# Kernel optimization log

Hardware: AMD Instinct MI355X
Metric: run time of the kernel (lower is better)

The kernel has to match this reference:

```python
import jax, jax.numpy as jnp
import numpy as np

DEPTH = 4
EPS = 1e-5


def block_pool(x, g):
    # adaptive max pool over a g x g grid of blocks, broadcast back to full size.
    # Equivalent to the recursive HalfSplit/adaptive_max_pool2d/QuarterStitch pyramid.
    B, C, H, W = x.shape
    xr = x.reshape(B, C, g, H // g, g, W // g)
    m = xr.max(axis=(3, 5), keepdims=True)          # [B,C,g,1,g,1]
    return jnp.broadcast_to(m, xr.shape).reshape(B, C, H, W)


def conv1x1_bn(x, w, gamma, beta):
    # Conv2DNormed: 1x1 conv (no bias) followed by BatchNorm (batch statistics).
    y = jnp.einsum('bchw,oc->bohw', x, w)
    mu = y.mean(axis=(0, 2, 3), keepdims=True)
    var = y.var(axis=(0, 2, 3), keepdims=True)
    yhat = (y - mu) * jax.lax.rsqrt(var + EPS)
    return yhat * gamma[None, :, None, None] + beta[None, :, None, None]


def setup_inputs() -> dict:
    key = jax.random.key(0)
    k0, k1, k2 = jax.random.split(key, 3)
    B, C, H, W = 4, 256, 192, 192
    x = jax.random.normal(k0, (B, C, H, W), jnp.float32)
    ws = jax.random.normal(k1, (DEPTH, C, C), jnp.float32) / np.float32(np.sqrt(C))
    gs = jnp.ones((DEPTH, C), jnp.float32)
    bs = jnp.zeros((DEPTH, C), jnp.float32)
    wf = jax.random.normal(k2, (C, (DEPTH + 1) * C), jnp.float32) / np.float32(np.sqrt((DEPTH + 1) * C))
    gf = jnp.ones((C,), jnp.float32)
    bf = jnp.zeros((C,), jnp.float32)
    return {"x": x, "ws": ws, "gs": gs, "bs": bs, "wf": wf, "gf": gf, "bf": bf}


def reference(x, ws, gs, bs, wf, gf, bf):
    # p[0] = raw input; p[1+d] = conv_d(block-pooled input at grid 2^d), d=0..DEPTH-1
    p = [x]
    for d in range(DEPTH):
        pooled = block_pool(x, 2 ** d)
        p.append(conv1x1_bn(pooled, ws[d], gs[d], bs[d]))
    out = jnp.concatenate(p, axis=1)                # [B, (DEPTH+1)*C, H, W]
    return conv1x1_bn(out, wf, gf, bf)
```

## Files before the change

### kernel.cpp

```cpp
#include <hip/hip_runtime.h>

typedef unsigned short u16;
typedef unsigned int   u32;
typedef __attribute__((ext_vector_type(4))) float f32x4;
typedef __attribute__((ext_vector_type(8))) short s16x8;
typedef __attribute__((ext_vector_type(4))) unsigned short u16x4;

#define HW    36864
#define WPIX  192
#define NCH   256
#define NB    4
#define NPIX  147456
#define POS   85
#define BN_EPS 1e-5f
#define NBKT  16

#define WS_PALL    0
#define WS_YD      (WS_PALL + NB*NCH*POS)
#define WS_PSUM    (WS_YD + NB*NCH*POS)
#define WS_PSQ     (WS_PSUM + 1024)
#define WS_PSC     (WS_PSQ + 1024)
#define WS_PBI     (WS_PSC + 1024)
#define WS_CONTRIB (WS_PBI + 1024)
#define WS_FSUMB   (WS_CONTRIB + NB*NCH*64)
#define WS_FSQB    (WS_FSUMB + NBKT*256)
#define WS_FSC     (WS_FSQB + NBKT*256)
#define WS_FBI     (WS_FSC + 256)
#define WS_WPK     (WS_FBI + 256)
#define WS_YBF     (WS_WPK + 32768)
#define WS_YBF_FLOATS (NB*NCH*HW/2)
#define WS_TOTAL   (WS_YBF + WS_YBF_FLOATS)

__device__ __forceinline__ u16 f2bf(float f) {
  u32 u = __builtin_bit_cast(u32, f);
  u += 0x7fffu + ((u >> 16) & 1u);
  return (u16)(u >> 16);
}
__device__ __forceinline__ float bf2f(u16 h) {
  u32 u = ((u32)h) << 16;
  return __builtin_bit_cast(float, u);
}

__global__ __launch_bounds__(192) void k_pool(const float* __restrict__ x, float* __restrict__ wsb) {
  __shared__ float sm[8][4][48];
  __shared__ float sp[84];
  int bc = blockIdx.x;
  const float* base = x + (size_t)bc * HW;
  int t = threadIdx.x;
  int cg = t % 48, rg = t / 48;
  if (bc == 0) {
    for (int i = t; i < 2048; i += 192) wsb[WS_PSUM + i] = 0.f;
    for (int i = t; i < 2*NBKT*256; i += 192) wsb[WS_FSUMB + i] = 0.f;
  }
  #pragma unroll
  for (int byi = 0; byi < 8; byi++) {
    float mm = -3.4e38f;
    #pragma unroll
    for (int rr = 0; rr < 6; rr++) {
      int r = byi*24 + rg + 4*rr;
      f32x4 v = *(const f32x4*)(base + r*WPIX + cg*4);
      mm = fmaxf(mm, fmaxf(fmaxf(v.x, v.y), fmaxf(v.z, v.w)));
    }
    sm[byi][rg][cg] = mm;
  }
  __syncthreads();
  size_t pb = WS_PALL + (size_t)bc * POS;
  if (t < 64) {
    int by = t >> 3, bx = t & 7;
    float mm = -3.4e38f;
    for (int r2 = 0; r2 < 4; r2++)
      for (int cq = 0; cq < 6; cq++)
        mm = fmaxf(mm, sm[by][r2][bx*6 + cq]);
    sp[t] = mm;
    wsb[pb + t] = mm;
  }
  __syncthreads();
  if (t < 16) {
    int i = t >> 2, j = t & 3;
    float mm = fmaxf(fmaxf(sp[(2*i)*8 + 2*j], sp[(2*i)*8 + 2*j + 1]),
                     fmaxf(sp[(2*i+1)*8 + 2*j], sp[(2*i+1)*8 + 2*j + 1]));
    sp[64 + t] = mm;
    wsb[pb + 64 + t] = mm;
  }
  __syncthreads();
  if (t < 4) {
    int i = t >> 1, j = t & 1;
    float mm = fmaxf(fmaxf(sp[64 + (2*i)*4 + 2*j], sp[64 + (2*i)*4 + 2*j + 1]),
                     fmaxf(sp[64 + (2*i+1)*4 + 2*j], sp[64 + (2*i+1)*4 + 2*j + 1]));
    sp[80 + t] = mm;
    wsb[pb + 80 + t] = mm;
  }
  __syncthreads();
  if (t == 0)
    wsb[pb + 84] = fmaxf(fmaxf(sp[80], sp[81]), fmaxf(sp[82], sp[83]));
}

__global__ __launch_bounds__(256) void k_wpack(const float* __restrict__ wf, float* __restrict__ wsb) {
  int fid = blockIdx.x*256 + threadIdx.x;
  int m = fid & 255, g = (fid >> 8) & 3, ks = fid >> 10;
  const float* src = wf + (size_t)m*1280 + ks*32 + g*8;
  f32x4 a = *(const f32x4*)src;
  f32x4 c = *(const f32x4*)(src + 4);
  u32* dst = (u32*)((u16*)(wsb + WS_WPK) + (size_t)fid*8);
  dst[0] = (u32)f2bf(a.x) | ((u32)f2bf(a.y) << 16);
  dst[1] = (u32)f2bf(a.z) | ((u32)f2bf(a.w) << 16);
  dst[2] = (u32)f2bf(c.x) | ((u32)f2bf(c.y) << 16);
  dst[3] = (u32)f2bf(c.z) | ((u32)f2bf(c.w) << 16);
}

__global__ __launch_bounds__(256) void k_pyr(const float* __restrict__ wconv, float* __restrict__ wsb) {
  __shared__ __align__(16) float pv[256];
  int bi = blockIdx.x;
  int b = bi / 85, pos = bi % 85;
  int d = (pos < 64) ? 3 : (pos < 80) ? 2 : (pos < 84) ? 1 : 0;
  int t = threadIdx.x;
  pv[t] = wsb[WS_PALL + (size_t)(b*NCH + t)*POS + pos];
  __syncthreads();
  const float* wrow = wconv + ((size_t)d*NCH + t)*NCH;
  float acc = 0.f;
  #pragma unroll 4
  for (int c4 = 0; c4 < 64; c4++) {
    f32x4 wv = *(const f32x4*)(wrow + c4*4);
    f32x4 xv = *(const f32x4*)(&pv[c4*4]);
    acc += wv.x*xv.x + wv.y*xv.y + wv.z*xv.z + wv.w*xv.w;
  }
  wsb[WS_YD + (size_t)(b*NCH + t)*POS + pos] = acc;
  atomicAdd(&wsb[WS_PSUM + d*NCH + t], acc);
  atomicAdd(&wsb[WS_PSQ  + d*NCH + t], acc*acc);
}

__global__ void k_pstats(const float* __restrict__ gs, const float* __restrict__ bs, float* __restrict__ wsb) {
  int t = blockIdx.x*256 + threadIdx.x;
  int d = t >> 8;
  float cnt = (float)(4 << (2*d));
  float mu  = wsb[WS_PSUM + t] / cnt;
  float var = wsb[WS_PSQ + t] / cnt - mu*mu;
  float sc  = gs[t] * rsqrtf(var + BN_EPS);
  wsb[WS_PSC + t] = sc;
  wsb[WS_PBI + t] = bs[t] - mu * sc;
}

__global__ __launch_bounds__(256) void k_contrib(const float* __restrict__ wf, float* __restrict__ wsb) {
  __shared__ __align__(16) float pn[1024];
  int bi = blockIdx.x;
  int b = bi >> 6, cell = bi & 63;
  int by = cell >> 3, bx = cell & 7;
  int t = threadIdx.x;
  int pos3 = cell;
  int pos2 = 64 + (by >> 1)*4 + (bx >> 1);
  int pos1 = 80 + (by >> 2)*2 + (bx >> 2);
  size_t yb = WS_YD + (size_t)(b*NCH + t)*POS;
  pn[0*NCH + t] = wsb[yb + 84]   * wsb[WS_PSC + 0*NCH + t] + wsb[WS_PBI + 0*NCH + t];
  pn[1*NCH + t] = wsb[yb + pos1] * wsb[WS_PSC + 1*NCH + t] + wsb[WS_PBI + 1*NCH + t];
  pn[2*NCH + t] = wsb[yb + pos2] * wsb[WS_PSC + 2*NCH + t] + wsb[WS_PBI + 2*NCH + t];
  pn[3*NCH + t] = wsb[yb + pos3] * wsb[WS_PSC + 3*NCH + t] + wsb[WS_PBI + 3*NCH + t];
  __syncthreads();
  const float* wrow = wf + (size_t)t*1280 + 256;
  float acc = 0.f;
  #pragma unroll 4
  for (int j = 0; j < 256; j++) {
    f32x4 wv = *(const f32x4*)(wrow + j*4);
    f32x4 xv = *(const f32x4*)(&pn[j*4]);
    acc += wv.x*xv.x + wv.y*xv.y + wv.z*xv.z + wv.w*xv.w;
  }
  wsb[WS_CONTRIB + (size_t)(b*NCH + t)*64 + cell] = acc;
}

template<bool YBF>
__global__ __launch_bounds__(256) void k_main(const float* __restrict__ x,
                                              float* __restrict__ wsb, float* __restrict__ y) {
  __shared__ __align__(16) u16 xlds[2][64*40];
  int wg = blockIdx.x;
  int b = wg / 576, nt = wg % 576;
  int pbase = nt * 64;
  int by8   = ((nt / 3) / 24) * 8;
  int wbase = (nt % 3) * 64;
  int t = threadIdx.x;
  int wave = t >> 6, l = t & 63;
  int g = l >> 4, ln = l & 15;
  int sn = t & 63;
  int kh = t >> 6;
  const float* xb = x + (size_t)b*NCH*HW + pbase + sn;
  const u16* wpk = (const u16*)(wsb + WS_WPK);
  int mrow = wave*64 + ln;

  f32x4 acc[4][4];
  #pragma unroll
  for (int i = 0; i < 4; i++)
    #pragma unroll
    for (int j = 0; j < 4; j++)
      acc[i][j] = {0.f, 0.f, 0.f, 0.f};

  float xr0[8], xr1[8];
  s16x8 a0[4], a1[4];

  #pragma unroll
  for (int j = 0; j < 8; j++) xr0[j] = xb[(size_t)(kh*8 + j)*HW];
  #pragma unroll
  for (int tm = 0; tm < 4; tm++)
    a0[tm] = *(const s16x8*)(wpk + ((size_t)(0*4 + g)*256 + mrow + tm*16)*8);

  #pragma unroll
  for (int ks = 0; ks < 8; ks++) {
    float    (&xr)[8] = (ks & 1) ? xr1 : xr0;
    s16x8    (&af)[4] = (ks & 1) ? a1  : a0;
    float    (&xrn)[8] = (ks & 1) ? xr0 : xr1;
    s16x8    (&afn)[4] = (ks & 1) ? a0  : a1;
    s16x8 pk;
    #pragma unroll
    for (int j = 0; j < 8; j++) pk[j] = (short)f2bf(xr[j]);
    *(s16x8*)(&xlds[ks & 1][sn*40 + kh*8]) = pk;
    __syncthreads();
    if (ks < 7) {
      #pragma unroll
      for (int j = 0; j < 8; j++) xrn[j] = xb[(size_t)((ks+1)*32 + kh*8 + j)*HW];
      #pragma unroll
      for (int tm = 0; tm < 4; tm++)
        afn[tm] = *(const s16x8*)(wpk + ((size_t)((ks+1)*4 + g)*256 + mrow + tm*16)*8);
    }
    #pragma unroll
    for (int tn = 0; tn < 4; tn++) {
      s16x8 bfr = *(const s16x8*)(&xlds[ks & 1][(tn*16 + ln)*40 + g*8]);
      #pragma unroll
      for (int tm = 0; tm < 4; tm++)
        acc[tm][tn] = __builtin_amdgcn_mfma_f32_16x16x32_bf16(af[tm], bfr, acc[tm][tn], 0, 0, 0);
    }
  }

  const float* cb = wsb + WS_CONTRIB + (size_t)b*NCH*64;
  int bkt = wg & (NBKT - 1);
  float* fsum = wsb + WS_FSUMB + bkt*256;
  float* fsq  = wsb + WS_FSQB  + bkt*256;
  u16*   ybb  = (u16*)(wsb + WS_YBF) + (size_t)b*NCH*HW + pbase;
  float* ybf32 = y + (size_t)b*NCH*HW + pbase;
  #pragma unroll
  for (int tm = 0; tm < 4; tm++) {
    int ob = wave*64 + tm*16 + g*4;
    #pragma unroll
    for (int r = 0; r < 4; r++) {
      int o = ob + r;
      float s1 = 0.f, s2 = 0.f;
      #pragma unroll
      for (int tn = 0; tn < 4; tn++) {
        int n = tn*16 + ln;
        int bx = (wbase + n) / 24;
        float yv = acc[tm][tn][r] + cb[(size_t)o*64 + by8 + bx];
        if (YBF) {
          u16 h = f2bf(yv);
          float yr = bf2f(h);
          ybb[(size_t)o*HW + n] = h;
          s1 += yr; s2 += yr*yr;
        } else {
          ybf32[(size_t)o*HW + n] = yv;
          s1 += yv; s2 += yv*yv;
        }
      }
      s1 += __shfl_xor(s1, 1);  s2 += __shfl_xor(s2, 1);
      s1 += __shfl_xor(s1, 2);  s2 += __shfl_xor(s2, 2);
      s1 += __shfl_xor(s1, 4);  s2 += __shfl_xor(s2, 4);
      s1 += __shfl_xor(s1, 8);  s2 += __shfl_xor(s2, 8);
      if (ln == 0) { atomicAdd(&fsum[o], s1); atomicAdd(&fsq[o], s2); }
    }
  }
}

__global__ void k_fstats(const float* __restrict__ gf, const float* __restrict__ bfv, float* __restrict__ wsb) {
  int o = threadIdx.x;
  float s1 = 0.f, s2 = 0.f;
  #pragma unroll
  for (int i = 0; i < NBKT; i++) {
    s1 += wsb[WS_FSUMB + i*256 + o];
    s2 += wsb[WS_FSQB  + i*256 + o];
  }
  float inv = 1.f / (float)NPIX;
  float mu  = s1 * inv;
  float var = s2 * inv - mu*mu;
  float sc  = gf[o] * rsqrtf(var + BN_EPS);
  wsb[WS_FSC + o] = sc;
  wsb[WS_FBI + o] = bfv[o] - mu * sc;
}

template<bool YBF>
__global__ __launch_bounds__(256) void k_norm(float* __restrict__ out, const float* __restrict__ wsb) {
  int bid = blockIdx.x;
  int plane = bid >> 2, q = bid & 3;
  int c = plane & 255;
  float sc = wsb[WS_FSC + c], bi = wsb[WS_FBI + c];
  size_t base4 = ((size_t)plane*HW + q*(HW/4)) >> 2;
  int t = threadIdx.x;
  if (YBF) {
    const u16* yb = (const u16*)(wsb + WS_YBF);
    #pragma unroll
    for (int it = 0; it < 9; it++) {
      size_t i4 = base4 + it*256 + t;
      u16x4 v = *(const u16x4*)(yb + i4*4);
      f32x4 o;
      o.x = bf2f(v.x)*sc + bi;
      o.y = bf2f(v.y)*sc + bi;
      o.z = bf2f(v.z)*sc + bi;
      o.w = bf2f(v.w)*sc + bi;
      ((f32x4*)out)[i4] = o;
    }
  } else {
    #pragma unroll
    for (int it = 0; it < 9; it++) {
      size_t i4 = base4 + it*256 + t;
      f32x4 v = ((f32x4*)out)[i4];
      v.x = v.x*sc + bi; v.y = v.y*sc + bi; v.z = v.z*sc + bi; v.w = v.w*sc + bi;
      ((f32x4*)out)[i4] = v;
    }
  }
}

extern "C" void kernel_launch(void* const* d_in, const int* in_sizes, int n_in,
                              void* d_out, int out_size, void* d_ws, size_t ws_size,
                              hipStream_t stream) {
  const float* x  = (const float*)d_in[0];
  const float* w  = (const float*)d_in[1];
  const float* gs = (const float*)d_in[2];
  const float* bs = (const float*)d_in[3];
  const float* wf = (const float*)d_in[4];
  const float* gf = (const float*)d_in[5];
  const float* bf = (const float*)d_in[6];
  float* y   = (float*)d_out;
  float* wsb = (float*)d_ws;

  bool ybf = ws_size >= (size_t)WS_TOTAL * sizeof(float);

  k_pool   <<<NB*NCH, 192, 0, stream>>>(x, wsb);
  k_wpack  <<<32, 256, 0, stream>>>(wf, wsb);
  k_pyr    <<<NB*POS, 256, 0, stream>>>(w, wsb);
  k_pstats <<<4, 256, 0, stream>>>(gs, bs, wsb);
  k_contrib<<<NB*64, 256, 0, stream>>>(wf, wsb);
  if (ybf) k_main<true> <<<NB*576, 256, 0, stream>>>(x, wsb, y);
  else     k_main<false><<<NB*576, 256, 0, stream>>>(x, wsb, y);
  k_fstats <<<1, 256, 0, stream>>>(gf, bf, wsb);
  if (ybf) k_norm<true> <<<4096, 256, 0, stream>>>(y, wsb);
  else     k_norm<false><<<4096, 256, 0, stream>>>(y, wsb);
}
```

Baseline: 200.4 us.

## Fuse BN stat kernels, batch contrib across images, restage main-kernel x loads

```diff
diff --git a/kernel.cpp b/kernel.cpp
--- a/kernel.cpp
+++ b/kernel.cpp
@@ -5,9 +5,9 @@
 typedef __attribute__((ext_vector_type(4))) float f32x4;
 typedef __attribute__((ext_vector_type(8))) short s16x8;
 typedef __attribute__((ext_vector_type(4))) unsigned short u16x4;
+typedef __attribute__((ext_vector_type(8))) unsigned short u16x8;
 
 #define HW    36864
-#define WPIX  192
 #define NCH   256
 #define NB    4
 #define NPIX  147456
@@ -16,20 +16,15 @@
 #define NBKT  16
 
 #define WS_PALL    0
-#define WS_YD      (WS_PALL + NB*NCH*POS)
-#define WS_PSUM    (WS_YD + NB*NCH*POS)
-#define WS_PSQ     (WS_PSUM + 1024)
-#define WS_PSC     (WS_PSQ + 1024)
-#define WS_PBI     (WS_PSC + 1024)
-#define WS_CONTRIB (WS_PBI + 1024)
-#define WS_FSUMB   (WS_CONTRIB + NB*NCH*64)
-#define WS_FSQB    (WS_FSUMB + NBKT*256)
-#define WS_FSC     (WS_FSQB + NBKT*256)
-#define WS_FBI     (WS_FSC + 256)
-#define WS_WPK     (WS_FBI + 256)
-#define WS_YBF     (WS_WPK + 32768)
-#define WS_YBF_FLOATS (NB*NCH*HW/2)
-#define WS_TOTAL   (WS_YBF + WS_YBF_FLOATS)
+#define WS_YD      87040
+#define WS_PSUM    174080
+#define WS_PSQ     175104
+#define WS_CONTRIB 176128
+#define WS_FSUMB   241664
+#define WS_FSQB    245760
+#define WS_WPK     249856
+#define WS_YBF     282624
+#define WS_TOT1    (WS_YBF + NB*NCH*HW/2)
 
 __device__ __forceinline__ u16 f2bf(float f) {
   u32 u = __builtin_bit_cast(u32, f);
@@ -50,7 +45,7 @@
   int cg = t % 48, rg = t / 48;
   if (bc == 0) {
     for (int i = t; i < 2048; i += 192) wsb[WS_PSUM + i] = 0.f;
-    for (int i = t; i < 2*NBKT*256; i += 192) wsb[WS_FSUMB + i] = 0.f;
+    for (int i = t; i < 8192; i += 192) wsb[WS_FSUMB + i] = 0.f;
   }
   #pragma unroll
   for (int byi = 0; byi < 8; byi++) {
@@ -58,7 +53,7 @@
     #pragma unroll
     for (int rr = 0; rr < 6; rr++) {
       int r = byi*24 + rg + 4*rr;
-      f32x4 v = *(const f32x4*)(base + r*WPIX + cg*4);
+      f32x4 v = *(const f32x4*)(base + r*192 + cg*4);
       mm = fmaxf(mm, fmaxf(fmaxf(v.x, v.y), fmaxf(v.z, v.w)));
     }
     sm[byi][rg][cg] = mm;
@@ -129,60 +124,95 @@
   atomicAdd(&wsb[WS_PSQ  + d*NCH + t], acc*acc);
 }
 
-__global__ void k_pstats(const float* __restrict__ gs, const float* __restrict__ bs, float* __restrict__ wsb) {
-  int t = blockIdx.x*256 + threadIdx.x;
-  int d = t >> 8;
-  float cnt = (float)(4 << (2*d));
-  float mu  = wsb[WS_PSUM + t] / cnt;
-  float var = wsb[WS_PSQ + t] / cnt - mu*mu;
-  float sc  = gs[t] * rsqrtf(var + BN_EPS);
-  wsb[WS_PSC + t] = sc;
-  wsb[WS_PBI + t] = bs[t] - mu * sc;
-}
-
-__global__ __launch_bounds__(256) void k_contrib(const float* __restrict__ wf, float* __restrict__ wsb) {
-  __shared__ __align__(16) float pn[1024];
-  int bi = blockIdx.x;
-  int b = bi >> 6, cell = bi & 63;
+__global__ __launch_bounds__(256) void k_contrib(const float* __restrict__ wf,
+                                                 const float* __restrict__ gs,
+                                                 const float* __restrict__ bs,
+                                                 float* __restrict__ wsb) {
+  __shared__ __align__(16) float pn[16][256];
+  int cell = blockIdx.x;
   int by = cell >> 3, bx = cell & 7;
   int t = threadIdx.x;
-  int pos3 = cell;
-  int pos2 = 64 + (by >> 1)*4 + (bx >> 1);
-  int pos1 = 80 + (by >> 2)*2 + (bx >> 2);
-  size_t yb = WS_YD + (size_t)(b*NCH + t)*POS;
-  pn[0*NCH + t] = wsb[yb + 84]   * wsb[WS_PSC + 0*NCH + t] + wsb[WS_PBI + 0*NCH + t];
-  pn[1*NCH + t] = wsb[yb + pos1] * wsb[WS_PSC + 1*NCH + t] + wsb[WS_PBI + 1*NCH + t];
-  pn[2*NCH + t] = wsb[yb + pos2] * wsb[WS_PSC + 2*NCH + t] + wsb[WS_PBI + 2*NCH + t];
-  pn[3*NCH + t] = wsb[yb + pos3] * wsb[WS_PSC + 3*NCH + t] + wsb[WS_PBI + 3*NCH + t];
-  __syncthreads();
-  const float* wrow = wf + (size_t)t*1280 + 256;
-  float acc = 0.f;
-  #pragma unroll 4
-  for (int j = 0; j < 256; j++) {
-    f32x4 wv = *(const f32x4*)(wrow + j*4);
-    f32x4 xv = *(const f32x4*)(&pn[j*4]);
-    acc += wv.x*xv.x + wv.y*xv.y + wv.z*xv.z + wv.w*xv.w;
-  }
-  wsb[WS_CONTRIB + (size_t)(b*NCH + t)*64 + cell] = acc;
+  #pragma unroll
+  for (int d = 0; d < 4; d++) {
+    int pos = (d == 3) ? cell
+            : (d == 2) ? 64 + (by >> 1)*4 + (bx >> 1)
+            : (d == 1) ? 80 + (by >> 2)*2 + (bx >> 2)
+            : 84;
+    float cnt = (float)(4 << (2*d));
+    float mu  = wsb[WS_PSUM + d*NCH + t] / cnt;
+    float var = wsb[WS_PSQ  + d*NCH + t] / cnt - mu*mu;
+    float sc  = gs[d*NCH + t] * rsqrtf(var + BN_EPS);
+    float bi_ = bs[d*NCH + t] - mu * sc;
+    #pragma unroll
+    for (int b = 0; b < 4; b++)
+      pn[d*4 + b][t] = wsb[WS_YD + (size_t)(b*NCH + t)*POS + pos] * sc + bi_;
+  }
+  __syncthreads();
+  float a0 = 0.f, a1 = 0.f, a2 = 0.f, a3 = 0.f;
+  #pragma unroll
+  for (int d = 0; d < 4; d++) {
+    const float* wrow = wf + (size_t)t*1280 + 256 + d*256;
+    #pragma unroll 4
+    for (int j = 0; j < 64; j++) {
+      f32x4 wv = *(const f32x4*)(wrow + j*4);
+      f32x4 p0 = *(const f32x4*)(&pn[d*4 + 0][j*4]);
+      f32x4 p1 = *(const f32x4*)(&pn[d*4 + 1][j*4]);
+      f32x4 p2 = *(const f32x4*)(&pn[d*4 + 2][j*4]);
+      f32x4 p3 = *(const f32x4*)(&pn[d*4 + 3][j*4]);
+      a0 += wv.x*p0.x + wv.y*p0.y + wv.z*p0.z + wv.w*p0.w;
+      a1 += wv.x*p1.x + wv.y*p1.y + wv.z*p1.z + wv.w*p1.w;
+      a2 += wv.x*p2.x + wv.y*p2.y + wv.z*p2.z + wv.w*p2.w;
+      a3 += wv.x*p3.x + wv.y*p3.y + wv.z*p3.z + wv.w*p3.w;
+    }
+  }
+  wsb[WS_CONTRIB + (size_t)(0*NCH + t)*64 + cell] = a0;
+  wsb[WS_CONTRIB + (size_t)(1*NCH + t)*64 + cell] = a1;
+  wsb[WS_CONTRIB + (size_t)(2*NCH + t)*64 + cell] = a2;
+  wsb[WS_CONTRIB + (size_t)(3*NCH + t)*64 + cell] = a3;
 }
 
 template<bool YBF>
-__global__ __launch_bounds__(256) void k_main(const float* __restrict__ x,
-                                              float* __restrict__ wsb, float* __restrict__ y) {
-  __shared__ __align__(16) u16 xlds[2][64*40];
+__global__ __launch_bounds__(256, 3) void k_main(const float* __restrict__ x,
+                                                 float* __restrict__ wsb, float* __restrict__ y) {
+  __shared__ __align__(16) u32 xbuf[2][64*20];
+  __shared__ float ctile[256*4];
   int wg = blockIdx.x;
-  int b = wg / 576, nt = wg % 576;
-  int pbase = nt * 64;
-  int by8   = ((nt / 3) / 24) * 8;
-  int wbase = (nt % 3) * 64;
-  int t = threadIdx.x;
-  int wave = t >> 6, l = t & 63;
-  int g = l >> 4, ln = l & 15;
-  int sn = t & 63;
-  int kh = t >> 6;
-  const float* xb = x + (size_t)b*NCH*HW + pbase + sn;
+  int b = wg / 576, tile = wg % 576;
+  int n0 = tile * 64;
+  int t = threadIdx.x, w = t >> 6, l = t & 63, g = l >> 4, ln = l & 15;
+  int cb0 = (tile % 3) * 64;
+  int rowblk = (tile / 3) / 24;
+  int cblk0 = cb0 / 24;
   const u16* wpk = (const u16*)(wsb + WS_WPK);
-  int mrow = wave*64 + ln;
+  int mrow = w*64 + ln;
+  int qq = t & 15, c2 = t >> 4;
+  const float* xsrc = x + (size_t)(b*NCH + 2*c2)*HW + n0 + 4*qq;
+
+  float ct[4];
+  {
+    const float* cbase = wsb + WS_CONTRIB + ((size_t)b*NCH + t)*64 + rowblk*8;
+    #pragma unroll
+    for (int i = 0; i < 4; i++) {
+      int cc = cblk0 + i; if (cc > 7) cc = 7;
+      ct[i] = cbase[cc];
+    }
+  }
+  f32x4 xa[4], xbv[4];
+  #pragma unroll
+  for (int i = 0; i < 4; i++) {
+    xa[i]  = *(const f32x4*)(xsrc + (size_t)(i*32)*HW);
+    xbv[i] = *(const f32x4*)(xsrc + (size_t)(i*32 + 1)*HW);
+  }
+  s16x8 af[2][4];
+  #pragma unroll
+  for (int tm = 0; tm < 4; tm++)
+    af[0][tm] = *(const s16x8*)(wpk + ((size_t)g*256 + mrow + tm*16)*8);
+
+  #pragma unroll
+  for (int i = 0; i < 4; i++) ctile[t*4 + i] = ct[i];
+  asm volatile("s_waitcnt lgkmcnt(0)" ::: "memory");
+  __builtin_amdgcn_s_barrier();
+  __builtin_amdgcn_sched_barrier(0);
 
   f32x4 acc[4][4];
   #pragma unroll
@@ -191,68 +221,69 @@
     for (int j = 0; j < 4; j++)
       acc[i][j] = {0.f, 0.f, 0.f, 0.f};
 
-  float xr0[8], xr1[8];
-  s16x8 a0[4], a1[4];
-
-  #pragma unroll
-  for (int j = 0; j < 8; j++) xr0[j] = xb[(size_t)(kh*8 + j)*HW];
-  #pragma unroll
-  for (int tm = 0; tm < 4; tm++)
-    a0[tm] = *(const s16x8*)(wpk + ((size_t)(0*4 + g)*256 + mrow + tm*16)*8);
-
-  #pragma unroll
-  for (int ks = 0; ks < 8; ks++) {
-    float    (&xr)[8] = (ks & 1) ? xr1 : xr0;
-    s16x8    (&af)[4] = (ks & 1) ? a1  : a0;
-    float    (&xrn)[8] = (ks & 1) ? xr0 : xr1;
-    s16x8    (&afn)[4] = (ks & 1) ? a0  : a1;
-    s16x8 pk;
-    #pragma unroll
-    for (int j = 0; j < 8; j++) pk[j] = (short)f2bf(xr[j]);
-    *(s16x8*)(&xlds[ks & 1][sn*40 + kh*8]) = pk;
-    __syncthreads();
-    if (ks < 7) {
+  int slot = (((c2 >> 2) ^ (qq & 3)) << 2) | (c2 & 3);
+
+  #pragma unroll
+  for (int i = 0; i < 8; i++) {
+    {
+      u32* dst = &xbuf[i & 1][0];
+      f32x4 va = xa[i & 3], vb = xbv[i & 3];
       #pragma unroll
-      for (int j = 0; j < 8; j++) xrn[j] = xb[(size_t)((ks+1)*32 + kh*8 + j)*HW];
+      for (int j = 0; j < 4; j++) {
+        u32 pk = (u32)f2bf(va[j]) | ((u32)f2bf(vb[j]) << 16);
+        dst[(4*qq + j)*20 + slot] = pk;
+      }
+    }
+    asm volatile("s_waitcnt lgkmcnt(0)" ::: "memory");
+    __builtin_amdgcn_s_barrier();
+    __builtin_amdgcn_sched_barrier(0);
+    if (i < 4) {
+      xa[i & 3]  = *(const f32x4*)(xsrc + (size_t)((i+4)*32)*HW);
+      xbv[i & 3] = *(const f32x4*)(xsrc + (size_t)((i+4)*32 + 1)*HW);
+    }
+    if (i < 7) {
       #pragma unroll
       for (int tm = 0; tm < 4; tm++)
-        afn[tm] = *(const s16x8*)(wpk + ((size_t)((ks+1)*4 + g)*256 + mrow + tm*16)*8);
+        af[(i+1) & 1][tm] = *(const s16x8*)(wpk + ((size_t)((i+1)*4 + g)*256 + mrow + tm*16)*8);
     }
     #pragma unroll
     for (int tn = 0; tn < 4; tn++) {
-      s16x8 bfr = *(const s16x8*)(&xlds[ks & 1][(tn*16 + ln)*40 + g*8]);
+      int px = 16*tn + ln;
+      int gr = g ^ ((px >> 2) & 3);
+      s16x8 bfr = *(const s16x8*)((const u16*)&xbuf[i & 1][px*20 + gr*4]);
       #pragma unroll
       for (int tm = 0; tm < 4; tm++)
-        acc[tm][tn] = __builtin_amdgcn_mfma_f32_16x16x32_bf16(af[tm], bfr, acc[tm][tn], 0, 0, 0);
-    }
-  }
-
-  const float* cb = wsb + WS_CONTRIB + (size_t)b*NCH*64;
+        acc[tm][tn] = __builtin_amdgcn_mfma_f32_16x16x32_bf16(af[i & 1][tm], bfr, acc[tm][tn], 0, 0, 0);
+    }
+  }
+
+  int ci[4];
+  #pragma unroll
+  for (int tn = 0; tn < 4; tn++)
+    ci[tn] = (cb0 + 16*tn + ln)/24 - cblk0;
   int bkt = wg & (NBKT - 1);
   float* fsum = wsb + WS_FSUMB + bkt*256;
   float* fsq  = wsb + WS_FSQB  + bkt*256;
-  u16*   ybb  = (u16*)(wsb + WS_YBF) + (size_t)b*NCH*HW + pbase;
-  float* ybf32 = y + (size_t)b*NCH*HW + pbase;
+  u16*   ybb  = (u16*)(wsb + WS_YBF) + (size_t)b*NCH*HW + n0;
+  float* yf   = y + (size_t)b*NCH*HW + n0;
   #pragma unroll
   for (int tm = 0; tm < 4; tm++) {
-    int ob = wave*64 + tm*16 + g*4;
     #pragma unroll
     for (int r = 0; r < 4; r++) {
-      int o = ob + r;
+      int o = w*64 + tm*16 + g*4 + r;
       float s1 = 0.f, s2 = 0.f;
       #pragma unroll
       for (int tn = 0; tn < 4; tn++) {
-        int n = tn*16 + ln;
-        int bx = (wbase + n) / 24;
-        float yv = acc[tm][tn][r] + cb[(size_t)o*64 + by8 + bx];
+        int px = 16*tn + ln;
+        float v = acc[tm][tn][r] + ctile[o*4 + ci[tn]];
         if (YBF) {
-          u16 h = f2bf(yv);
+          u16 h = f2bf(v);
+          ybb[(size_t)o*HW + px] = h;
           float yr = bf2f(h);
-          ybb[(size_t)o*HW + n] = h;
           s1 += yr; s2 += yr*yr;
         } else {
-          ybf32[(size_t)o*HW + n] = yv;
-          s1 += yv; s2 += yv*yv;
+          yf[(size_t)o*HW + px] = v;
+          s1 += v; s2 += v*v;
         }
       }
       s1 += __shfl_xor(s1, 1);  s2 += __shfl_xor(s2, 1);
@@ -264,44 +295,56 @@
   }
 }
 
-__global__ void k_fstats(const float* __restrict__ gf, const float* __restrict__ bfv, float* __restrict__ wsb) {
-  int o = threadIdx.x;
-  float s1 = 0.f, s2 = 0.f;
-  #pragma unroll
-  for (int i = 0; i < NBKT; i++) {
-    s1 += wsb[WS_FSUMB + i*256 + o];
-    s2 += wsb[WS_FSQB  + i*256 + o];
-  }
-  float inv = 1.f / (float)NPIX;
-  float mu  = s1 * inv;
-  float var = s2 * inv - mu*mu;
-  float sc  = gf[o] * rsqrtf(var + BN_EPS);
-  wsb[WS_FSC + o] = sc;
-  wsb[WS_FBI + o] = bfv[o] - mu * sc;
-}
-
 template<bool YBF>
-__global__ __launch_bounds__(256) void k_norm(float* __restrict__ out, const float* __restrict__ wsb) {
+__global__ __launch_bounds__(256) void k_norm(float* __restrict__ out,
+                                              const float* __restrict__ gf,
+                                              const float* __restrict__ bfv,
+                                              const float* __restrict__ wsb) {
   int bid = blockIdx.x;
-  int plane = bid >> 2, q = bid & 3;
-  int c = plane & 255;
-  float sc = wsb[WS_FSC + c], bi = wsb[WS_FBI + c];
-  size_t base4 = ((size_t)plane*HW + q*(HW/4)) >> 2;
   int t = threadIdx.x;
   if (YBF) {
+    int plane = bid >> 1, hf = bid & 1;
+    int c = plane & 255;
+    float s1 = 0.f, s2 = 0.f;
+    #pragma unroll
+    for (int i = 0; i < NBKT; i++) {
+      s1 += wsb[WS_FSUMB + i*256 + c];
+      s2 += wsb[WS_FSQB  + i*256 + c];
+    }
+    float inv = 1.f / (float)NPIX;
+    float mu  = s1 * inv;
+    float var = s2 * inv - mu*mu;
+    float sc  = gf[c] * rsqrtf(var + BN_EPS);
+    float bi  = bfv[c] - mu * sc;
     const u16* yb = (const u16*)(wsb + WS_YBF);
+    size_t gbase = (size_t)plane*4608 + hf*2304;
     #pragma unroll
     for (int it = 0; it < 9; it++) {
-      size_t i4 = base4 + it*256 + t;
-      u16x4 v = *(const u16x4*)(yb + i4*4);
-      f32x4 o;
-      o.x = bf2f(v.x)*sc + bi;
-      o.y = bf2f(v.y)*sc + bi;
-      o.z = bf2f(v.z)*sc + bi;
-      o.w = bf2f(v.w)*sc + bi;
-      ((f32x4*)out)[i4] = o;
+      size_t gi = gbase + it*256 + t;
+      u16x8 v = *(const u16x8*)(yb + gi*8);
+      f32x4 o0, o1;
+      o0.x = bf2f(v[0])*sc + bi; o0.y = bf2f(v[1])*sc + bi;
+      o0.z = bf2f(v[2])*sc + bi; o0.w = bf2f(v[3])*sc + bi;
+      o1.x = bf2f(v[4])*sc + bi; o1.y = bf2f(v[5])*sc + bi;
+      o1.z = bf2f(v[6])*sc + bi; o1.w = bf2f(v[7])*sc + bi;
+      ((f32x4*)out)[gi*2]     = o0;
+      ((f32x4*)out)[gi*2 + 1] = o1;
     }
   } else {
+    int plane = bid >> 2, q = bid & 3;
+    int c = plane & 255;
+    float s1 = 0.f, s2 = 0.f;
+    #pragma unroll
+    for (int i = 0; i < NBKT; i++) {
+      s1 += wsb[WS_FSUMB + i*256 + c];
+      s2 += wsb[WS_FSQB  + i*256 + c];
+    }
+    float inv = 1.f / (float)NPIX;
+    float mu  = s1 * inv;
+    float var = s2 * inv - mu*mu;
+    float sc  = gf[c] * rsqrtf(var + BN_EPS);
+    float bi  = bfv[c] - mu * sc;
+    size_t base4 = ((size_t)plane*HW + q*(HW/4)) >> 2;
     #pragma unroll
     for (int it = 0; it < 9; it++) {
       size_t i4 = base4 + it*256 + t;
@@ -325,16 +368,14 @@
   float* y   = (float*)d_out;
   float* wsb = (float*)d_ws;
 
-  bool ybf = ws_size >= (size_t)WS_TOTAL * sizeof(float);
+  bool ybf = ws_size >= (size_t)WS_TOT1 * sizeof(float);
 
   k_pool   <<<NB*NCH, 192, 0, stream>>>(x, wsb);
   k_wpack  <<<32, 256, 0, stream>>>(wf, wsb);
   k_pyr    <<<NB*POS, 256, 0, stream>>>(w, wsb);
-  k_pstats <<<4, 256, 0, stream>>>(gs, bs, wsb);
-  k_contrib<<<NB*64, 256, 0, stream>>>(wf, wsb);
+  k_contrib<<<64, 256, 0, stream>>>(wf, gs, bs, wsb);
   if (ybf) k_main<true> <<<NB*576, 256, 0, stream>>>(x, wsb, y);
   else     k_main<false><<<NB*576, 256, 0, stream>>>(x, wsb, y);
-  k_fstats <<<1, 256, 0, stream>>>(gf, bf, wsb);
-  if (ybf) k_norm<true> <<<4096, 256, 0, stream>>>(y, wsb);
-  else     k_norm<false><<<4096, 256, 0, stream>>>(y, wsb);
-}
+  if (ybf) k_norm<true> <<<2048, 256, 0, stream>>>(y, gf, bf, wsb);
+  else     k_norm<false><<<4096, 256, 0, stream>>>(y, gf, bf, wsb);
+}
```

Measured after the change: 213.3 us. +6.4%, slower.
